# Performance work log

Measured on AMD Instinct MI355X. Metric: run time of the kernel, lower is better.

The kernel has to match this reference:

```python
import jax, jax.numpy as jnp
import numpy as np

D, M, ALPHA = 64, 512, 7.18
DIM = 1024
B = M * D  # batch: M clusters x D samples each


def setup_inputs() -> dict:
    key = jax.random.key(0)
    outputs = jax.random.normal(key, (B, DIM), dtype=jnp.float32)
    indices = jnp.arange(B, dtype=jnp.int64 if jax.config.jax_enable_x64 else jnp.int32)
    assignment = indices // D  # sample i -> cluster i//D (contiguous blocks of D)
    loss_vector = jnp.zeros((M,), jnp.float32)
    loss_count = jnp.zeros((M,), jnp.float32)
    return {"outputs": outputs, "indices": indices, "assignment": assignment,
            "loss_vector": loss_vector, "loss_count": loss_count}


def reference(outputs, indices, assignment, loss_vector, loss_count):
    outputs = outputs.astype(jnp.float32)
    own = assignment[indices]                              # [B] cluster id per sample
    n = jnp.float32(B)
    # cluster means (each cluster has exactly D samples)
    means = jax.ops.segment_sum(outputs, own, num_segments=M) / D   # [M, DIM]
    # pooled variance: sum ||x_i - mu_{c(i)}||^2 / (N - 1)
    diff_own = outputs - means[own]
    var_sum = jnp.sum(diff_own * diff_own)
    stdev = -2.0 * var_sum / (n - 1.0)                     # the (negative) -2*sigma^2 term
    # squared distances to every cluster mean: [B, M]
    sq = (jnp.sum(outputs * outputs, axis=1)[:, None]
          + jnp.sum(means * means, axis=1)[None, :]
          - 2.0 * outputs @ means.T)
    exps = jnp.exp(sq / stdev)                             # [B, M]
    own_col = own[:, None]
    own_exp = jnp.take_along_axis(exps, own_col, axis=1)[:, 0]
    denom = jnp.sum(exps, axis=1) - own_exp                # sum over mF != own
    sq_own = jnp.take_along_axis(sq, own_col, axis=1)[:, 0]
    log_ratio = sq_own / stdev - ALPHA - jnp.log(denom)    # log(exp(.-alpha)/denom)
    per_loss = jnp.maximum(-log_ratio, 0.0)                # == -clamp(log_ratio, max=0)
    loss = (jnp.sum(per_loss) / n).reshape(1)
    lv = (loss_vector + jax.ops.segment_sum(per_loss, own, num_segments=M)) / n
    lc = loss_count + jax.ops.segment_sum(jnp.ones((B,), jnp.float32), own, num_segments=M)
    variance = var_sum / (n - 1.0)                         # stdev / -2.0 in the original
    return loss, lv, lc, variance
```

## Files before the change

### kernel.cpp

```cpp
#include <hip/hip_runtime.h>
#include <hip/hip_bf16.h>
#include <stdint.h>

#define DIM 1024
#define ALPHA 7.18f
#define INV_N (1.0f/32768.0f)
#define NM1 32767.0f
#define LOG2E 1.44269504088896f
#define LN2 0.693147180559945f

typedef __attribute__((ext_vector_type(8))) short bfrag8;
typedef __attribute__((ext_vector_type(4))) float f32x4;

typedef const __attribute__((address_space(1))) void gv_t;
typedef __attribute__((address_space(3))) void lv_t;

__device__ __forceinline__ unsigned f2bf_bits(float f) {
    unsigned u = __float_as_uint(f);
    return (u + 0x7fffu + ((u >> 16) & 1u)) >> 16;
}

__global__ __launch_bounds__(1024)
void k1_colsum(const float* __restrict__ outputs, const int* __restrict__ indices,
               const int* __restrict__ assignment, float* __restrict__ mean_sums,
               unsigned* __restrict__ counts, float* __restrict__ scalars,
               int* __restrict__ own_g) {
    __shared__ int sown[64];
    __shared__ float swsum[16];
    const int d = threadIdx.x;
    const int row0 = blockIdx.x * 64;
    if (d < 64) {
        int m = assignment[indices[row0 + d]];
        sown[d] = m;
        own_g[row0 + d] = m;
        atomicAdd(&counts[m], 1u);
    }
    __syncthreads();
    const float* p = outputs + (size_t)row0 * DIM + d;
    float msum = 0.f, ssum = 0.f;
    int curm = sown[0];
    #pragma unroll 8
    for (int r = 0; r < 64; ++r) {
        float o = p[(size_t)r * DIM];
        ssum = fmaf(o, o, ssum);
        int m = sown[r];
        if (m != curm) {
            atomicAdd(&mean_sums[(size_t)curm * DIM + d], msum);
            msum = 0.f; curm = m;
        }
        msum += o;
    }
    atomicAdd(&mean_sums[(size_t)curm * DIM + d], msum);
    #pragma unroll
    for (int mk = 32; mk; mk >>= 1) ssum += __shfl_xor(ssum, mk, 64);
    if ((d & 63) == 0) swsum[d >> 6] = ssum;
    __syncthreads();
    if (d == 0) {
        float s = 0.f;
        #pragma unroll
        for (int w = 0; w < 16; ++w) s += swsum[w];
        atomicAdd(&scalars[0], s);
    }
}

__global__ __launch_bounds__(256)
void k2_means(const float* __restrict__ mean_sums, const unsigned* __restrict__ counts,
              unsigned short* __restrict__ means_bf, float* __restrict__ msq,
              float* __restrict__ scalars) {
    const int m = blockIdx.x, t = threadIdx.x;
    const float* row = mean_sums + (size_t)m * DIM;
    unsigned short* ob = means_bf + (size_t)m * DIM;
    float sq = 0.f;
    #pragma unroll
    for (int i = 0; i < 4; ++i) {
        int dcol = t + i * 256;
        float mu = row[dcol] * (1.0f / 64.0f);
        ob[dcol] = (unsigned short)f2bf_bits(mu);
        sq = fmaf(mu, mu, sq);
    }
    #pragma unroll
    for (int mk = 32; mk; mk >>= 1) sq += __shfl_xor(sq, mk, 64);
    __shared__ float sw[4];
    if ((t & 63) == 0) sw[t >> 6] = sq;
    __syncthreads();
    if (t == 0) {
        float s = sw[0] + sw[1] + sw[2] + sw[3];
        msq[m] = s;
        atomicAdd(&scalars[1], ((float)counts[m] - 128.0f) * s);
    }
}

__global__ __launch_bounds__(512)
void k3_finalize(float* __restrict__ scalars, const float* __restrict__ msq,
                 const unsigned* __restrict__ counts, const float* __restrict__ loss_vector,
                 const float* __restrict__ loss_count, float* __restrict__ msl,
                 float* __restrict__ out) {
    const int t = threadIdx.x;
    float var_sum = scalars[0] + scalars[1];
    float inv_std = -NM1 / (2.0f * var_sum);
    msl[t] = msq[t] * inv_std * LOG2E;
    out[1 + t] = loss_vector[t] * INV_N;
    out[513 + t] = loss_count[t] + (float)counts[t];
    if (t == 0) {
        out[0] = 0.0f;
        out[1025] = var_sum / NM1;
        scalars[2] = inv_std;
    }
}

__global__ __launch_bounds__(512)
void k4_gemm(const float* __restrict__ outputs, const unsigned short* __restrict__ means_bf,
             const float* __restrict__ msl, const float* __restrict__ scalars,
             const int* __restrict__ own_g, float* __restrict__ out) {
    __shared__ short lA[2][64 * 32];
    __shared__ short lB[2][512 * 32];
    __shared__ float red_sum[64][4];
    __shared__ float red_own[64][4];

    const int tid  = threadIdx.x;
    const int lane = tid & 63;
    const int wid  = tid >> 6;
    const int wm   = wid >> 2;
    const int wn   = wid & 3;
    const int brow = blockIdx.x * 64;

    const int rA = tid >> 3;
    const int kq = tid & 7;
    const float* gA = outputs + (size_t)(brow + rA) * DIM + kq * 4;
    const int aw_byte = rA * 64 + (((kq >> 1) ^ ((rA >> 1) & 3)) << 4) + ((kq & 1) << 3);

    const int mB = lane >> 2;
    const int pB = lane & 3;

    const int arow = wm * 32 + (lane & 15);
    const int ar_byte = arow * 64 + (((lane >> 4) ^ ((arow >> 1) & 3)) << 4);
    const int bcol = wn * 128 + (lane & 15);
    const int br_byte = bcol * 64 + (((lane >> 4) ^ ((bcol >> 1) & 3)) << 4);

    f32x4 acc[2][8];
    #pragma unroll
    for (int i = 0; i < 2; ++i)
        #pragma unroll
        for (int j = 0; j < 8; ++j)
            acc[i][j] = (f32x4){0.f, 0.f, 0.f, 0.f};

    {
        #pragma unroll
        for (int i = 0; i < 4; ++i) {
            int m = (wid * 4 + i) * 16 + mB;
            int s = pB ^ ((m >> 1) & 3);
            const char* gsrc = (const char*)means_bf + (size_t)m * 2048 + s * 16;
            char* ldst = (char*)&lB[0][0] + (wid * 4 + i) * 1024;
            __builtin_amdgcn_global_load_lds((gv_t*)gsrc, (lv_t*)ldst, 16, 0, 0);
        }
        float4 areg = *(const float4*)gA;
        unsigned lo = f2bf_bits(areg.x) | (f2bf_bits(areg.y) << 16);
        unsigned hi = f2bf_bits(areg.z) | (f2bf_bits(areg.w) << 16);
        *(uint2*)((char*)&lA[0][0] + aw_byte) = make_uint2(lo, hi);
    }
    __syncthreads();

    int cur = 0;
    for (int t = 0; t < 32; ++t) {
        const bool has_next = (t + 1) < 32;
        float4 anext;
        if (has_next) {
            anext = *(const float4*)(gA + (t + 1) * 32);
            #pragma unroll
            for (int i = 0; i < 4; ++i) {
                int m = (wid * 4 + i) * 16 + mB;
                int s = pB ^ ((m >> 1) & 3);
                const char* gsrc = (const char*)means_bf + (size_t)m * 2048
                                   + (size_t)(t + 1) * 64 + s * 16;
                char* ldst = (char*)&lB[cur ^ 1][0] + (wid * 4 + i) * 1024;
                __builtin_amdgcn_global_load_lds((gv_t*)gsrc, (lv_t*)ldst, 16, 0, 0);
            }
        }
        const char* pa = (const char*)&lA[cur][0] + ar_byte;
        const char* pb = (const char*)&lB[cur][0] + br_byte;
        bfrag8 a0 = *(const bfrag8*)(pa);
        bfrag8 a1 = *(const bfrag8*)(pa + 1024);
        #pragma unroll
        for (int fn = 0; fn < 8; ++fn) {
            bfrag8 bf = *(const bfrag8*)(pb + fn * 1024);
            acc[0][fn] = __builtin_amdgcn_mfma_f32_16x16x32_bf16(a0, bf, acc[0][fn], 0, 0, 0);
            acc[1][fn] = __builtin_amdgcn_mfma_f32_16x16x32_bf16(a1, bf, acc[1][fn], 0, 0, 0);
        }
        if (has_next) {
            unsigned lo = f2bf_bits(anext.x) | (f2bf_bits(anext.y) << 16);
            unsigned hi = f2bf_bits(anext.z) | (f2bf_bits(anext.w) << 16);
            *(uint2*)((char*)&lA[cur ^ 1][0] + aw_byte) = make_uint2(lo, hi);
        }
        __syncthreads();
        cur ^= 1;
    }

    float mslv[8];
    #pragma unroll
    for (int fn = 0; fn < 8; ++fn) mslv[fn] = msl[bcol + fn * 16];
    const float inv_std = scalars[2];
    const float c2k = -2.0f * inv_std * LOG2E;
    int ownv[2][4];
    #pragma unroll
    for (int fm = 0; fm < 2; ++fm)
        #pragma unroll
        for (int rg = 0; rg < 4; ++rg)
            ownv[fm][rg] = own_g[brow + wm * 32 + fm * 16 + ((lane >> 4) << 2) + rg];

    #pragma unroll
    for (int fm = 0; fm < 2; ++fm) {
        #pragma unroll
        for (int rg = 0; rg < 4; ++rg) {
            float sum = 0.f, oa = -1e30f;
            int ownr = ownv[fm][rg];
            #pragma unroll
            for (int fn = 0; fn < 8; ++fn) {
                float dot = acc[fm][fn][rg];
                float arg = fmaf(c2k, dot, mslv[fn]);
                sum += exp2f(arg);
                bool isown = (bcol + fn * 16) == ownr;
                oa = isown ? arg : oa;
            }
            #pragma unroll
            for (int mk = 1; mk < 16; mk <<= 1) {
                sum += __shfl_xor(sum, mk, 64);
                oa = fmaxf(oa, __shfl_xor(oa, mk, 64));
            }
            if ((lane & 15) == 0) {
                int r_in = wm * 32 + fm * 16 + ((lane >> 4) << 2) + rg;
                red_sum[r_in][wn] = sum;
                red_own[r_in][wn] = oa;
            }
        }
    }
    __syncthreads();

    if (tid < 64) {
        float s = red_sum[tid][0] + red_sum[tid][1] + red_sum[tid][2] + red_sum[tid][3];
        float oa = fmaxf(fmaxf(red_own[tid][0], red_own[tid][1]),
                         fmaxf(red_own[tid][2], red_own[tid][3]));
        float denom = s - exp2f(oa);
        float per_loss = fmaxf(ALPHA + LN2 * (log2f(denom) - oa), 0.f);
        int ownr = own_g[brow + tid];
        float ls = per_loss;
        #pragma unroll
        for (int mk = 1; mk < 64; mk <<= 1) ls += __shfl_xor(ls, mk, 64);
        int own0 = __shfl(ownr, 0, 64);
        if (__all(ownr == own0)) {
            if (tid == 0) atomicAdd(&out[1 + own0], ls * INV_N);
        } else {
            atomicAdd(&out[1 + ownr], per_loss * INV_N);
        }
        if (tid == 0) atomicAdd(&out[0], ls * INV_N);
    }
}

extern "C" void kernel_launch(void* const* d_in, const int* in_sizes, int n_in,
                              void* d_out, int out_size, void* d_ws, size_t ws_size,
                              hipStream_t stream) {
    const float* outputs     = (const float*)d_in[0];
    const int*   indices     = (const int*)d_in[1];
    const int*   assignment  = (const int*)d_in[2];
    const float* loss_vector = (const float*)d_in[3];
    const float* loss_count  = (const float*)d_in[4];
    float* out = (float*)d_out;

    char* ws = (char*)d_ws;
    float*          mean_sums = (float*)ws;
    unsigned*       counts    = (unsigned*)(ws + 2097152);
    float*          scalars   = (float*)(ws + 2097152 + 2048);
    const size_t    ZB        = 2097152 + 2048 + 256;
    unsigned short* means_bf  = (unsigned short*)(ws + 2101248);
    float*          msq       = (float*)(ws + 2101248 + 1048576);
    float*          msl       = (float*)(ws + 2101248 + 1048576 + 2048);
    int*            own_g     = (int*)(ws + 2101248 + 1048576 + 4096);

    hipMemsetAsync(d_ws, 0, ZB, stream);
    hipLaunchKernelGGL(k1_colsum, dim3(512), dim3(1024), 0, stream,
                       outputs, indices, assignment, mean_sums, counts, scalars, own_g);
    hipLaunchKernelGGL(k2_means, dim3(512), dim3(256), 0, stream,
                       mean_sums, counts, means_bf, msq, scalars);
    hipLaunchKernelGGL(k3_finalize, dim3(1), dim3(512), 0, stream,
                       scalars, msq, counts, loss_vector, loss_count, msl, out);
    hipLaunchKernelGGL(k4_gemm, dim3(512), dim3(512), 0, stream,
                       outputs, means_bf, msl, scalars, own_g, out);
}
```

Measured before the change: 322.2 us.

## Pre-convert outputs to swizzled bf16 in colsum and stream tiles via direct LDS loads

The column-sum kernel now also writes a bf16 copy of outputs, pre-swizzled in the GEMM's LDS tile layout, into a 64 MB workspace region. It also gains a uniform-cluster fast path with float4 loads. The means are likewise stored k-tile-major and pre-swizzled, so the GEMM fetches both A and B tiles with contiguous global_load_lds and no per-iteration fp32 loads or conversions. The GEMM then reads half as many A bytes, at the cost of an extra 64 MB write in k1. A fallback path keeps the old scheme when the workspace is too small.

```diff
diff --git a/kernel.cpp b/kernel.cpp
--- a/kernel.cpp
+++ b/kernel.cpp
@@ -20,64 +20,113 @@
     return (u + 0x7fffu + ((u >> 16) & 1u)) >> 16;
 }
 
-__global__ __launch_bounds__(1024)
+template<int APRIME>
+__global__ __launch_bounds__(512)
 void k1_colsum(const float* __restrict__ outputs, const int* __restrict__ indices,
                const int* __restrict__ assignment, float* __restrict__ mean_sums,
                unsigned* __restrict__ counts, float* __restrict__ scalars,
-               int* __restrict__ own_g) {
+               int* __restrict__ own_g, unsigned short* __restrict__ a_bf) {
     __shared__ int sown[64];
-    __shared__ float swsum[16];
-    const int d = threadIdx.x;
+    __shared__ int suni;
+    __shared__ float4 spart[256];
+    __shared__ float ssq[8];
+    const int tid = threadIdx.x;
     const int row0 = blockIdx.x * 64;
-    if (d < 64) {
-        int m = assignment[indices[row0 + d]];
-        sown[d] = m;
-        own_g[row0 + d] = m;
+    if (tid == 0) suni = 1;
+    if (tid < 64) {
+        int m = assignment[indices[row0 + tid]];
+        sown[tid] = m;
+        own_g[row0 + tid] = m;
         atomicAdd(&counts[m], 1u);
     }
     __syncthreads();
-    const float* p = outputs + (size_t)row0 * DIM + d;
-    float msum = 0.f, ssum = 0.f;
-    int curm = sown[0];
-    #pragma unroll 8
-    for (int r = 0; r < 64; ++r) {
-        float o = p[(size_t)r * DIM];
-        ssum = fmaf(o, o, ssum);
-        int m = sown[r];
-        if (m != curm) {
-            atomicAdd(&mean_sums[(size_t)curm * DIM + d], msum);
-            msum = 0.f; curm = m;
-        }
-        msum += o;
-    }
-    atomicAdd(&mean_sums[(size_t)curm * DIM + d], msum);
-    #pragma unroll
-    for (int mk = 32; mk; mk >>= 1) ssum += __shfl_xor(ssum, mk, 64);
-    if ((d & 63) == 0) swsum[d >> 6] = ssum;
-    __syncthreads();
-    if (d == 0) {
+    if (tid < 63 && sown[tid] != sown[tid + 1]) suni = 0;
+    __syncthreads();
+
+    const int c4 = tid & 255;
+    const int rh = tid >> 8;
+    const float* gp = outputs + (size_t)(row0 + rh * 32) * DIM + c4 * 4;
+    const int tt = c4 >> 3, kc = (c4 >> 1) & 3, half = c4 & 1;
+    char* abase = (char*)a_bf + (size_t)blockIdx.x * 131072 + tt * 4096 + half * 8;
+
+    float4 s4 = {0.f, 0.f, 0.f, 0.f};
+    float sq = 0.f;
+    if (suni) {
+        #pragma unroll 8
+        for (int r = 0; r < 32; ++r) {
+            float4 v = *(const float4*)(gp + (size_t)r * DIM);
+            sq = fmaf(v.x, v.x, sq); sq = fmaf(v.y, v.y, sq);
+            sq = fmaf(v.z, v.z, sq); sq = fmaf(v.w, v.w, sq);
+            s4.x += v.x; s4.y += v.y; s4.z += v.z; s4.w += v.w;
+            if (APRIME) {
+                int rr = rh * 32 + r;
+                unsigned lo = f2bf_bits(v.x) | (f2bf_bits(v.y) << 16);
+                unsigned hi = f2bf_bits(v.z) | (f2bf_bits(v.w) << 16);
+                *(uint2*)(abase + rr * 64 + ((kc ^ ((rr >> 1) & 3)) << 4)) = make_uint2(lo, hi);
+            }
+        }
+        if (rh) spart[c4] = s4;
+        __syncthreads();
+        if (!rh) {
+            float4 o = spart[c4];
+            float* dst = mean_sums + (size_t)sown[0] * DIM + c4 * 4;
+            atomicAdd(dst + 0, s4.x + o.x);
+            atomicAdd(dst + 1, s4.y + o.y);
+            atomicAdd(dst + 2, s4.z + o.z);
+            atomicAdd(dst + 3, s4.w + o.w);
+        }
+    } else {
+        int curm = sown[rh * 32];
+        for (int r = 0; r < 32; ++r) {
+            int rr = rh * 32 + r;
+            float4 v = *(const float4*)(gp + (size_t)r * DIM);
+            int m = sown[rr];
+            if (m != curm) {
+                float* dst = mean_sums + (size_t)curm * DIM + c4 * 4;
+                atomicAdd(dst + 0, s4.x); atomicAdd(dst + 1, s4.y);
+                atomicAdd(dst + 2, s4.z); atomicAdd(dst + 3, s4.w);
+                s4 = (float4){0.f, 0.f, 0.f, 0.f};
+                curm = m;
+            }
+            sq = fmaf(v.x, v.x, sq); sq = fmaf(v.y, v.y, sq);
+            sq = fmaf(v.z, v.z, sq); sq = fmaf(v.w, v.w, sq);
+            s4.x += v.x; s4.y += v.y; s4.z += v.z; s4.w += v.w;
+            if (APRIME) {
+                unsigned lo = f2bf_bits(v.x) | (f2bf_bits(v.y) << 16);
+                unsigned hi = f2bf_bits(v.z) | (f2bf_bits(v.w) << 16);
+                *(uint2*)(abase + rr * 64 + ((kc ^ ((rr >> 1) & 3)) << 4)) = make_uint2(lo, hi);
+            }
+        }
+        float* dst = mean_sums + (size_t)curm * DIM + c4 * 4;
+        atomicAdd(dst + 0, s4.x); atomicAdd(dst + 1, s4.y);
+        atomicAdd(dst + 2, s4.z); atomicAdd(dst + 3, s4.w);
+    }
+    #pragma unroll
+    for (int mk = 32; mk; mk >>= 1) sq += __shfl_xor(sq, mk, 64);
+    if ((tid & 63) == 0) ssq[tid >> 6] = sq;
+    __syncthreads();
+    if (tid == 0) {
         float s = 0.f;
         #pragma unroll
-        for (int w = 0; w < 16; ++w) s += swsum[w];
+        for (int w = 0; w < 8; ++w) s += ssq[w];
         atomicAdd(&scalars[0], s);
     }
 }
 
 __global__ __launch_bounds__(256)
 void k2_means(const float* __restrict__ mean_sums, const unsigned* __restrict__ counts,
-              unsigned short* __restrict__ means_bf, float* __restrict__ msq,
+              unsigned short* __restrict__ b_kt, float* __restrict__ msq,
               float* __restrict__ scalars) {
     const int m = blockIdx.x, t = threadIdx.x;
     const float* row = mean_sums + (size_t)m * DIM;
-    unsigned short* ob = means_bf + (size_t)m * DIM;
-    float sq = 0.f;
-    #pragma unroll
-    for (int i = 0; i < 4; ++i) {
-        int dcol = t + i * 256;
-        float mu = row[dcol] * (1.0f / 64.0f);
-        ob[dcol] = (unsigned short)f2bf_bits(mu);
-        sq = fmaf(mu, mu, sq);
-    }
+    float4 v = *(const float4*)(row + t * 4);
+    float4 mu = {v.x * (1.0f/64.0f), v.y * (1.0f/64.0f), v.z * (1.0f/64.0f), v.w * (1.0f/64.0f)};
+    const int tt = t >> 3, kc = (t >> 1) & 3, half = t & 1;
+    unsigned lo = f2bf_bits(mu.x) | (f2bf_bits(mu.y) << 16);
+    unsigned hi = f2bf_bits(mu.z) | (f2bf_bits(mu.w) << 16);
+    *(uint2*)((char*)b_kt + tt * 32768 + m * 64 + ((kc ^ ((m >> 1) & 3)) << 4) + half * 8)
+        = make_uint2(lo, hi);
+    float sq = fmaf(mu.x, mu.x, fmaf(mu.y, mu.y, fmaf(mu.z, mu.z, mu.w * mu.w)));
     #pragma unroll
     for (int mk = 32; mk; mk >>= 1) sq += __shfl_xor(sq, mk, 64);
     __shared__ float sw[4];
@@ -108,10 +157,12 @@
     }
 }
 
+template<int APRIME>
 __global__ __launch_bounds__(512)
-void k4_gemm(const float* __restrict__ outputs, const unsigned short* __restrict__ means_bf,
-             const float* __restrict__ msl, const float* __restrict__ scalars,
-             const int* __restrict__ own_g, float* __restrict__ out) {
+void k4_gemm(const float* __restrict__ outputs, const unsigned short* __restrict__ a_bf,
+             const unsigned short* __restrict__ b_kt, const float* __restrict__ msl,
+             const float* __restrict__ scalars, const int* __restrict__ own_g,
+             float* __restrict__ out) {
     __shared__ short lA[2][64 * 32];
     __shared__ short lB[2][512 * 32];
     __shared__ float red_sum[64][4];
@@ -129,14 +180,14 @@
     const float* gA = outputs + (size_t)(brow + rA) * DIM + kq * 4;
     const int aw_byte = rA * 64 + (((kq >> 1) ^ ((rA >> 1) & 3)) << 4) + ((kq & 1) << 3);
 
-    const int mB = lane >> 2;
-    const int pB = lane & 3;
-
     const int arow = wm * 32 + (lane & 15);
     const int ar_byte = arow * 64 + (((lane >> 4) ^ ((arow >> 1) & 3)) << 4);
     const int bcol = wn * 128 + (lane & 15);
     const int br_byte = bcol * 64 + (((lane >> 4) ^ ((bcol >> 1) & 3)) << 4);
 
+    const char* aprime = (const char*)a_bf + (size_t)blockIdx.x * 131072;
+    const char* bbase  = (const char*)b_kt;
+
     f32x4 acc[2][8];
     #pragma unroll
     for (int i = 0; i < 2; ++i)
@@ -144,15 +195,19 @@
         for (int j = 0; j < 8; ++j)
             acc[i][j] = (f32x4){0.f, 0.f, 0.f, 0.f};
 
-    {
-        #pragma unroll
-        for (int i = 0; i < 4; ++i) {
-            int m = (wid * 4 + i) * 16 + mB;
-            int s = pB ^ ((m >> 1) & 3);
-            const char* gsrc = (const char*)means_bf + (size_t)m * 2048 + s * 16;
-            char* ldst = (char*)&lB[0][0] + (wid * 4 + i) * 1024;
+    #pragma unroll
+    for (int i = 0; i < 4; ++i) {
+        const char* gsrc = bbase + (wid * 4 + i) * 1024 + lane * 16;
+        char* ldst = (char*)&lB[0][0] + (wid * 4 + i) * 1024;
+        __builtin_amdgcn_global_load_lds((gv_t*)gsrc, (lv_t*)ldst, 16, 0, 0);
+    }
+    if (APRIME) {
+        if (wid < 4) {
+            const char* gsrc = aprime + wid * 1024 + lane * 16;
+            char* ldst = (char*)&lA[0][0] + wid * 1024;
             __builtin_amdgcn_global_load_lds((gv_t*)gsrc, (lv_t*)ldst, 16, 0, 0);
         }
+    } else {
         float4 areg = *(const float4*)gA;
         unsigned lo = f2bf_bits(areg.x) | (f2bf_bits(areg.y) << 16);
         unsigned hi = f2bf_bits(areg.z) | (f2bf_bits(areg.w) << 16);
@@ -163,19 +218,25 @@
     int cur = 0;
     for (int t = 0; t < 32; ++t) {
         const bool has_next = (t + 1) < 32;
-        float4 anext;
         if (has_next) {
-            anext = *(const float4*)(gA + (t + 1) * 32);
             #pragma unroll
             for (int i = 0; i < 4; ++i) {
-                int m = (wid * 4 + i) * 16 + mB;
-                int s = pB ^ ((m >> 1) & 3);
-                const char* gsrc = (const char*)means_bf + (size_t)m * 2048
-                                   + (size_t)(t + 1) * 64 + s * 16;
+                const char* gsrc = bbase + (size_t)(t + 1) * 32768 + (wid * 4 + i) * 1024 + lane * 16;
                 char* ldst = (char*)&lB[cur ^ 1][0] + (wid * 4 + i) * 1024;
                 __builtin_amdgcn_global_load_lds((gv_t*)gsrc, (lv_t*)ldst, 16, 0, 0);
             }
         }
+        float4 anext;
+        if (APRIME) {
+            if (has_next && wid < 4) {
+                const char* gsrc = aprime + (size_t)(t + 1) * 4096 + wid * 1024 + lane * 16;
+                char* ldst = (char*)&lA[cur ^ 1][0] + wid * 1024;
+                __builtin_amdgcn_global_load_lds((gv_t*)gsrc, (lv_t*)ldst, 16, 0, 0);
+            }
+        } else if (has_next) {
+            anext = *(const float4*)(gA + (t + 1) * 32);
+        }
+
         const char* pa = (const char*)&lA[cur][0] + ar_byte;
         const char* pb = (const char*)&lB[cur][0] + br_byte;
         bfrag8 a0 = *(const bfrag8*)(pa);
@@ -186,7 +247,8 @@
             acc[0][fn] = __builtin_amdgcn_mfma_f32_16x16x32_bf16(a0, bf, acc[0][fn], 0, 0, 0);
             acc[1][fn] = __builtin_amdgcn_mfma_f32_16x16x32_bf16(a1, bf, acc[1][fn], 0, 0, 0);
         }
-        if (has_next) {
+
+        if (!APRIME && has_next) {
             unsigned lo = f2bf_bits(anext.x) | (f2bf_bits(anext.y) << 16);
             unsigned hi = f2bf_bits(anext.z) | (f2bf_bits(anext.w) << 16);
             *(uint2*)((char*)&lA[cur ^ 1][0] + aw_byte) = make_uint2(lo, hi);
@@ -268,20 +330,34 @@
     char* ws = (char*)d_ws;
     float*          mean_sums = (float*)ws;
     unsigned*       counts    = (unsigned*)(ws + 2097152);
-    float*          scalars   = (float*)(ws + 2097152 + 2048);
-    const size_t    ZB        = 2097152 + 2048 + 256;
-    unsigned short* means_bf  = (unsigned short*)(ws + 2101248);
-    float*          msq       = (float*)(ws + 2101248 + 1048576);
-    float*          msl       = (float*)(ws + 2101248 + 1048576 + 2048);
-    int*            own_g     = (int*)(ws + 2101248 + 1048576 + 4096);
+    float*          scalars   = (float*)(ws + 2099200);
+    const size_t    ZB        = 2099456;
+    unsigned short* b_kt      = (unsigned short*)(ws + 2101248);
+    float*          msq       = (float*)(ws + 3149824);
+    float*          msl       = (float*)(ws + 3151872);
+    int*            own_g     = (int*)(ws + 3153920);
+    const size_t    A_OFF     = 4194304;
+    unsigned short* a_bf      = (unsigned short*)(ws + A_OFF);
+    const size_t    NEED      = A_OFF + 67108864ULL;
 
     hipMemsetAsync(d_ws, 0, ZB, stream);
-    hipLaunchKernelGGL(k1_colsum, dim3(512), dim3(1024), 0, stream,
-                       outputs, indices, assignment, mean_sums, counts, scalars, own_g);
-    hipLaunchKernelGGL(k2_means, dim3(512), dim3(256), 0, stream,
-                       mean_sums, counts, means_bf, msq, scalars);
-    hipLaunchKernelGGL(k3_finalize, dim3(1), dim3(512), 0, stream,
-                       scalars, msq, counts, loss_vector, loss_count, msl, out);
-    hipLaunchKernelGGL(k4_gemm, dim3(512), dim3(512), 0, stream,
-                       outputs, means_bf, msl, scalars, own_g, out);
-}
+    if (ws_size >= NEED) {
+        hipLaunchKernelGGL((k1_colsum<1>), dim3(512), dim3(512), 0, stream,
+                           outputs, indices, assignment, mean_sums, counts, scalars, own_g, a_bf);
+        hipLaunchKernelGGL(k2_means, dim3(512), dim3(256), 0, stream,
+                           mean_sums, counts, b_kt, msq, scalars);
+        hipLaunchKernelGGL(k3_finalize, dim3(1), dim3(512), 0, stream,
+                           scalars, msq, counts, loss_vector, loss_count, msl, out);
+        hipLaunchKernelGGL((k4_gemm<1>), dim3(512), dim3(512), 0, stream,
+                           outputs, a_bf, b_kt, msl, scalars, own_g, out);
+    } else {
+        hipLaunchKernelGGL((k1_colsum<0>), dim3(512), dim3(512), 0, stream,
+                           outputs, indices, assignment, mean_sums, counts, scalars, own_g, a_bf);
+        hipLaunchKernelGGL(k2_means, dim3(512), dim3(256), 0, stream,
+                           mean_sums, counts, b_kt, msq, scalars);
+        hipLaunchKernelGGL(k3_finalize, dim3(1), dim3(512), 0, stream,
+                           scalars, msq, counts, loss_vector, loss_count, msl, out);
+        hipLaunchKernelGGL((k4_gemm<0>), dim3(512), dim3(512), 0, stream,
+                           outputs, a_bf, b_kt, msl, scalars, own_g, out);
+    }
+}
```

New measurement: 279.5 us. 13.3% less time.
